# Kernel tuning notes

Measured on AMD Instinct MI355X. Metric: run time of the kernel, lower is better.

Reference implementation:

```python
import jax, jax.numpy as jnp
import numpy as np

NUM_NODES = 17185
D = 6
FEATS = NUM_NODES * D  # 103110
BATCH = 256
EPS = 1e-5


def setup_inputs() -> dict:
    key = jax.random.key(0)
    ks = jax.random.split(key, 4)
    data = jax.random.normal(ks[0], (BATCH, FEATS), dtype=jnp.float32)
    w_blocks = jax.random.normal(ks[1], (NUM_NODES, D, D), dtype=jnp.float32) * (1.0 / np.sqrt(D))
    b_blocks = jax.random.normal(ks[2], (NUM_NODES, D), dtype=jnp.float32) * 0.1
    fc_w = jax.random.normal(ks[3], (FEATS,), dtype=jnp.float32) * (1.0 / np.sqrt(FEATS))
    return {
        "data": data,
        "w_blocks": w_blocks,
        "b_blocks": b_blocks,
        "bn_gamma": jnp.ones((FEATS,), jnp.float32),
        "bn_beta": jnp.zeros((FEATS,), jnp.float32),
        "bn_mean": jnp.zeros((FEATS,), jnp.float32),
        "bn_var": jnp.ones((FEATS,), jnp.float32),
        "fc_w": fc_w,
        "fc_b": jnp.zeros((1,), jnp.float32),
        "bnf_gamma": jnp.ones((1,), jnp.float32),
        "bnf_beta": jnp.zeros((1,), jnp.float32),
        "bnf_mean": jnp.zeros((1,), jnp.float32),
        "bnf_var": jnp.ones((1,), jnp.float32),
    }


def reference(data, w_blocks, b_blocks, bn_gamma, bn_beta, bn_mean, bn_var,
              fc_w, fc_b, bnf_gamma, bnf_beta, bnf_mean, bnf_var):
    B = data.shape[0]
    # block-diagonal batched matmul replacing 17185 tiny Linear(6,6) calls
    x = data.reshape(B, NUM_NODES, D)                       # [B, N, 6]
    xo = jnp.einsum("bni,noi->bno", x, w_blocks) + b_blocks  # torch Linear: x @ W^T + b
    xo = xo.reshape(B, FEATS)                               # hstack ordering == reshape
    # relu -> BatchNorm1d (eval: running stats) -> dropout (identity in eval)
    h = jnp.maximum(xo, 0.0)
    h = (h - bn_mean) * jax.lax.rsqrt(bn_var + EPS) * bn_gamma + bn_beta
    # final linear [FEATS -> 1], BN(1), sigmoid
    y = h @ fc_w + fc_b                                     # [B]
    y = y[:, None]                                          # [B, 1]
    y = (y - bnf_mean) * jax.lax.rsqrt(bnf_var + EPS) * bnf_gamma + bnf_beta
    return jax.nn.sigmoid(y)
```

## Files before the change

kernel.cpp:

```cpp
#include <hip/hip_runtime.h>
#include <stdint.h>

#define NUM_NODES 17185
#define DD 6
#define FEATS (NUM_NODES * DD)
#define BATCH 256
#define EPS 1e-5f

#define NC 256
#define BC 16
#define NCHUNK ((NUM_NODES + NC - 1) / NC)


__global__ __launch_bounds__(NC) void main_kernel(
    const float* __restrict__ data, const float* __restrict__ wb, const float* __restrict__ bb,
    const float* __restrict__ gamma, const float* __restrict__ var, const float* __restrict__ fcw,
    const float* __restrict__ beta, const float* __restrict__ mean,
    float* __restrict__ pm, float* __restrict__ pc) {

    const int tid = threadIdx.x;
    const int n = blockIdx.x * NC + tid;
    const bool valid = (n < NUM_NODES);

    float wreg[36], bias[6], a[6];
    #pragma unroll
    for (int k = 0; k < 36; k++) wreg[k] = 0.f;
    #pragma unroll
    for (int k = 0; k < 6; k++) { bias[k] = 0.f; a[k] = 0.f; }

    float cnode = 0.f;

    if (valid) {
        const float4* wp = (const float4*)(wb + (size_t)n * 36);
        #pragma unroll
        for (int k = 0; k < 9; k++) {
            float4 v = wp[k];
            wreg[4*k] = v.x; wreg[4*k+1] = v.y; wreg[4*k+2] = v.z; wreg[4*k+3] = v.w;
        }
        const float2* bp = (const float2*)(bb + (size_t)n * 6);
        #pragma unroll
        for (int k = 0; k < 3; k++) { float2 v = bp[k]; bias[2*k] = v.x; bias[2*k+1] = v.y; }
        const int f0 = n * 6;
        const float2* gp = (const float2*)(gamma + f0);
        const float2* vp = (const float2*)(var + f0);
        const float2* fp = (const float2*)(fcw + f0);
        float fw[6];
        #pragma unroll
        for (int k = 0; k < 3; k++) {
            float2 g = gp[k], v = vp[k], f = fp[k];
            fw[2*k] = f.x; fw[2*k+1] = f.y;
            a[2*k]   = g.x * rsqrtf(v.x + EPS) * f.x;
            a[2*k+1] = g.y * rsqrtf(v.y + EPS) * f.y;
        }
        if (blockIdx.y == 0) {
            const float2* bep = (const float2*)(beta + f0);
            const float2* mp  = (const float2*)(mean + f0);
            #pragma unroll
            for (int k = 0; k < 3; k++) {
                float2 be = bep[k], m = mp[k];
                cnode += be.x * fw[2*k]   - m.x * a[2*k];
                cnode += be.y * fw[2*k+1] - m.y * a[2*k+1];
            }
        }
    }

    const int b0 = blockIdx.y * BC;
    float acc[BC];
    #pragma unroll
    for (int r = 0; r < BC; r++) acc[r] = 0.f;

    if (valid) {
        const float2* xbase = (const float2*)(data + (size_t)b0 * FEATS + (size_t)n * 6);
        #pragma unroll
        for (int r = 0; r < BC; r++) {
            const float2* xp = xbase + (size_t)r * (FEATS / 2);
            float2 u0 = xp[0], u1 = xp[1], u2 = xp[2];
            float x0 = u0.x, x1 = u0.y, x2 = u1.x, x3 = u1.y, x4 = u2.x, x5 = u2.y;
            #pragma unroll
            for (int o = 0; o < 6; o++) {
                float s = bias[o];
                s = fmaf(x0, wreg[o*6+0], s);
                s = fmaf(x1, wreg[o*6+1], s);
                s = fmaf(x2, wreg[o*6+2], s);
                s = fmaf(x3, wreg[o*6+3], s);
                s = fmaf(x4, wreg[o*6+4], s);
                s = fmaf(x5, wreg[o*6+5], s);
                acc[r] = fmaf(fmaxf(s, 0.f), a[o], acc[r]);
            }
        }
    }

    __shared__ float red[4][BC];
    #pragma unroll
    for (int r = 0; r < BC; r++) {
        float v = acc[r];
        #pragma unroll
        for (int off = 32; off; off >>= 1) v += __shfl_down(v, off);
        if ((tid & 63) == 0) red[tid >> 6][r] = v;
    }

    if (blockIdx.y == 0) {
        float v = cnode;
        #pragma unroll
        for (int off = 32; off; off >>= 1) v += __shfl_down(v, off);
        __shared__ float credd[4];
        if ((tid & 63) == 0) credd[tid >> 6] = v;
        __syncthreads();
        if (tid == 0) pc[blockIdx.x] = credd[0] + credd[1] + credd[2] + credd[3];
    } else {
        __syncthreads();
    }

    if (tid < BC) {
        float s = red[0][tid] + red[1][tid] + red[2][tid] + red[3][tid];
        pm[blockIdx.x * 256 + b0 + tid] = s;
    }
}

__global__ __launch_bounds__(256) void final_kernel(
    const float* __restrict__ pm, const float* __restrict__ pc,
    const float* __restrict__ fcb, const float* __restrict__ bnfg,
    const float* __restrict__ bnfb, const float* __restrict__ bnfm,
    const float* __restrict__ bnfv, float* __restrict__ out) {
    const int b = threadIdx.x;

    float c = (b < NCHUNK) ? pc[b] : 0.f;
    #pragma unroll
    for (int off = 32; off; off >>= 1) c += __shfl_down(c, off);
    __shared__ float red[4];
    if ((b & 63) == 0) red[b >> 6] = c;
    __syncthreads();
    const float c_sum = red[0] + red[1] + red[2] + red[3];

    float y = 0.f;
    #pragma unroll 4
    for (int ch = 0; ch < NCHUNK; ch++) y += pm[ch * 256 + b];

    y += c_sum + fcb[0];
    float sc = bnfg[0] * rsqrtf(bnfv[0] + EPS);
    float z = (y - bnfm[0]) * sc + bnfb[0];
    out[b] = 1.f / (1.f + expf(-z));
}

extern "C" void kernel_launch(void* const* d_in, const int* in_sizes, int n_in,
                              void* d_out, int out_size, void* d_ws, size_t ws_size,
                              hipStream_t stream) {
    const float* data  = (const float*)d_in[0];
    const float* wb    = (const float*)d_in[1];
    const float* bb    = (const float*)d_in[2];
    const float* gamma = (const float*)d_in[3];
    const float* beta  = (const float*)d_in[4];
    const float* mean  = (const float*)d_in[5];
    const float* var   = (const float*)d_in[6];
    const float* fcw   = (const float*)d_in[7];
    const float* fcb   = (const float*)d_in[8];
    const float* bnfg  = (const float*)d_in[9];
    const float* bnfb  = (const float*)d_in[10];
    const float* bnfm  = (const float*)d_in[11];
    const float* bnfv  = (const float*)d_in[12];

    float* pm = (float*)d_ws;
    float* pc = pm + NCHUNK * 256;

    dim3 grid(NCHUNK, BATCH / BC);
    main_kernel<<<grid, NC, 0, stream>>>(data, wb, bb, gamma, var, fcw, beta, mean, pm, pc);

    final_kernel<<<1, 256, 0, stream>>>(pm, pc, fcb, bnfg, bnfb, bnfm, bnfv, (float*)d_out);
}
```

Baseline: 191.5 us.

## Add prep kernel for coalesced weights and stage data rows through swizzled LDS

A new prep kernel folds the BN scale and fc weights into per-node coefficients. It writes the weights, bias and folded coefficients into a global scratch buffer in structure-of-arrays float4 layout, so the main kernel reads them with coalesced loads. The main kernel now loads data rows with fully coalesced float2 accesses into a double-buffered, XOR-swizzled LDS tile, two rows per step, with register prefetch of the next rows. The goal is to replace the strided 24-byte-per-thread global reads. The cost is an extra kernel launch, extra scratch traffic and more barriers.

After: 201.7 us. 1.05x slower.

```diff
diff --git a/kernel.cpp b/kernel.cpp
--- a/kernel.cpp
+++ b/kernel.cpp
@@ -10,71 +10,137 @@
 #define NC 256
 #define BC 16
 #define NCHUNK ((NUM_NODES + NC - 1) / NC)
-
-
-__global__ __launch_bounds__(NC) void main_kernel(
-    const float* __restrict__ data, const float* __restrict__ wb, const float* __restrict__ bb,
-    const float* __restrict__ gamma, const float* __restrict__ var, const float* __restrict__ fcw,
-    const float* __restrict__ beta, const float* __restrict__ mean,
-    float* __restrict__ pm, float* __restrict__ pc) {
-
-    const int tid = threadIdx.x;
-    const int n = blockIdx.x * NC + tid;
+#define ROW_F2 (FEATS / 2)
+#define CHUNK_F2 768
+#define NIT (BC / 2)
+
+__device__ float4 g_W4[NCHUNK * 9 * 256];
+__device__ float4 g_P4[NCHUNK * 3 * 256];
+
+__device__ __forceinline__ int sw2(int i) { return i ^ (((i >> 4) & 7) << 1); }
+
+__global__ __launch_bounds__(256) void prep_kernel(
+    const float* __restrict__ wb, const float* __restrict__ bb,
+    const float* __restrict__ gamma, const float* __restrict__ var,
+    const float* __restrict__ fcw, const float* __restrict__ beta,
+    const float* __restrict__ mean, float* __restrict__ pc) {
+    const int t = threadIdx.x, c = blockIdx.x;
+    const int n = c * NC + t;
     const bool valid = (n < NUM_NODES);
 
-    float wreg[36], bias[6], a[6];
-    #pragma unroll
-    for (int k = 0; k < 36; k++) wreg[k] = 0.f;
-    #pragma unroll
-    for (int k = 0; k < 6; k++) { bias[k] = 0.f; a[k] = 0.f; }
-
-    float cnode = 0.f;
+    float w[36], bi[6], av[6];
+    #pragma unroll
+    for (int k = 0; k < 36; k++) w[k] = 0.f;
+    #pragma unroll
+    for (int k = 0; k < 6; k++) { bi[k] = 0.f; av[k] = 0.f; }
+    float cn = 0.f;
 
     if (valid) {
         const float4* wp = (const float4*)(wb + (size_t)n * 36);
         #pragma unroll
         for (int k = 0; k < 9; k++) {
             float4 v = wp[k];
-            wreg[4*k] = v.x; wreg[4*k+1] = v.y; wreg[4*k+2] = v.z; wreg[4*k+3] = v.w;
+            w[4*k] = v.x; w[4*k+1] = v.y; w[4*k+2] = v.z; w[4*k+3] = v.w;
         }
         const float2* bp = (const float2*)(bb + (size_t)n * 6);
         #pragma unroll
-        for (int k = 0; k < 3; k++) { float2 v = bp[k]; bias[2*k] = v.x; bias[2*k+1] = v.y; }
+        for (int k = 0; k < 3; k++) { float2 v = bp[k]; bi[2*k] = v.x; bi[2*k+1] = v.y; }
         const int f0 = n * 6;
-        const float2* gp = (const float2*)(gamma + f0);
-        const float2* vp = (const float2*)(var + f0);
-        const float2* fp = (const float2*)(fcw + f0);
-        float fw[6];
+        const float2* gp  = (const float2*)(gamma + f0);
+        const float2* vp  = (const float2*)(var + f0);
+        const float2* fp  = (const float2*)(fcw + f0);
+        const float2* bep = (const float2*)(beta + f0);
+        const float2* mp  = (const float2*)(mean + f0);
         #pragma unroll
         for (int k = 0; k < 3; k++) {
-            float2 g = gp[k], v = vp[k], f = fp[k];
-            fw[2*k] = f.x; fw[2*k+1] = f.y;
-            a[2*k]   = g.x * rsqrtf(v.x + EPS) * f.x;
-            a[2*k+1] = g.y * rsqrtf(v.y + EPS) * f.y;
-        }
-        if (blockIdx.y == 0) {
-            const float2* bep = (const float2*)(beta + f0);
-            const float2* mp  = (const float2*)(mean + f0);
+            float2 g = gp[k], v = vp[k], f = fp[k], be = bep[k], m = mp[k];
+            float a0 = g.x * rsqrtf(v.x + EPS) * f.x;
+            float a1 = g.y * rsqrtf(v.y + EPS) * f.y;
+            av[2*k] = a0; av[2*k+1] = a1;
+            cn += be.x * f.x - m.x * a0;
+            cn += be.y * f.y - m.y * a1;
+        }
+    }
+
+    float4* W4 = g_W4 + c * (9 * 256) + t;
+    #pragma unroll
+    for (int j = 0; j < 9; j++)
+        W4[j * 256] = make_float4(w[4*j], w[4*j+1], w[4*j+2], w[4*j+3]);
+    float4* P4 = g_P4 + c * (3 * 256) + t;
+    #pragma unroll
+    for (int k = 0; k < 3; k++)
+        P4[k * 256] = make_float4(bi[2*k], bi[2*k+1], av[2*k], av[2*k+1]);
+
+    #pragma unroll
+    for (int off = 32; off; off >>= 1) cn += __shfl_down(cn, off);
+    __shared__ float credd[4];
+    if ((t & 63) == 0) credd[t >> 6] = cn;
+    __syncthreads();
+    if (t == 0) pc[c] = credd[0] + credd[1] + credd[2] + credd[3];
+}
+
+__global__ __launch_bounds__(256) void main_kernel(
+    const float* __restrict__ data, float* __restrict__ pm) {
+    const int t = threadIdx.x, c = blockIdx.x;
+    const int b0 = blockIdx.y * BC;
+
+    float wreg[36], bias[6], a6[6];
+    {
+        const float4* W4 = g_W4 + c * (9 * 256) + t;
+        #pragma unroll
+        for (int j = 0; j < 9; j++) {
+            float4 v = W4[j * 256];
+            wreg[4*j] = v.x; wreg[4*j+1] = v.y; wreg[4*j+2] = v.z; wreg[4*j+3] = v.w;
+        }
+        const float4* P4 = g_P4 + c * (3 * 256) + t;
+        #pragma unroll
+        for (int k = 0; k < 3; k++) {
+            float4 v = P4[k * 256];
+            bias[2*k] = v.x; bias[2*k+1] = v.y; a6[2*k] = v.z; a6[2*k+1] = v.w;
+        }
+    }
+
+    __shared__ float2 lds2[2 * 1536];
+    const int maxf2 = (c == NCHUNK - 1) ? (ROW_F2 - c * CHUNK_F2) : CHUNK_F2;
+    const float2* dbase = (const float2*)data + (size_t)c * CHUNK_F2;
+
+    float acc[BC];
+    #pragma unroll
+    for (int r = 0; r < BC; r++) acc[r] = 0.f;
+
+    float2 st[6];
+    #pragma unroll
+    for (int k = 0; k < 6; k++) {
+        const int rr = (k >= 3);
+        const int off = t + 256 * (k - 3 * rr);
+        st[k] = (off < maxf2) ? dbase[(size_t)(b0 + rr) * ROW_F2 + off]
+                              : make_float2(0.f, 0.f);
+    }
+    #pragma unroll
+    for (int k = 0; k < 6; k++) {
+        const int idx = t + 256 * k;
+        lds2[sw2(idx)] = st[k];
+    }
+    __syncthreads();
+
+    #pragma unroll
+    for (int it = 0; it < NIT; ++it) {
+        if (it < NIT - 1) {
             #pragma unroll
-            for (int k = 0; k < 3; k++) {
-                float2 be = bep[k], m = mp[k];
-                cnode += be.x * fw[2*k]   - m.x * a[2*k];
-                cnode += be.y * fw[2*k+1] - m.y * a[2*k+1];
+            for (int k = 0; k < 6; k++) {
+                const int rr = (k >= 3);
+                const int off = t + 256 * (k - 3 * rr);
+                st[k] = (off < maxf2)
+                      ? dbase[(size_t)(b0 + 2 * (it + 1) + rr) * ROW_F2 + off]
+                      : make_float2(0.f, 0.f);
             }
         }
-    }
-
-    const int b0 = blockIdx.y * BC;
-    float acc[BC];
-    #pragma unroll
-    for (int r = 0; r < BC; r++) acc[r] = 0.f;
-
-    if (valid) {
-        const float2* xbase = (const float2*)(data + (size_t)b0 * FEATS + (size_t)n * 6);
-        #pragma unroll
-        for (int r = 0; r < BC; r++) {
-            const float2* xp = xbase + (size_t)r * (FEATS / 2);
-            float2 u0 = xp[0], u1 = xp[1], u2 = xp[2];
+        #pragma unroll
+        for (int r2 = 0; r2 < 2; r2++) {
+            const int base = (it & 1) * 1536 + 768 * r2 + 3 * t;
+            float2 u0 = lds2[sw2(base)];
+            float2 u1 = lds2[sw2(base + 1)];
+            float2 u2 = lds2[sw2(base + 2)];
             float x0 = u0.x, x1 = u0.y, x2 = u1.x, x3 = u1.y, x4 = u2.x, x5 = u2.y;
             #pragma unroll
             for (int o = 0; o < 6; o++) {
@@ -85,9 +151,17 @@
                 s = fmaf(x3, wreg[o*6+3], s);
                 s = fmaf(x4, wreg[o*6+4], s);
                 s = fmaf(x5, wreg[o*6+5], s);
-                acc[r] = fmaf(fmaxf(s, 0.f), a[o], acc[r]);
+                acc[2*it + r2] = fmaf(fmaxf(s, 0.f), a6[o], acc[2*it + r2]);
             }
         }
+        if (it < NIT - 1) {
+            #pragma unroll
+            for (int k = 0; k < 6; k++) {
+                const int idx = ((it + 1) & 1) * 1536 + t + 256 * k;
+                lds2[sw2(idx)] = st[k];
+            }
+        }
+        __syncthreads();
     }
 
     __shared__ float red[4][BC];
@@ -96,24 +170,12 @@
         float v = acc[r];
         #pragma unroll
         for (int off = 32; off; off >>= 1) v += __shfl_down(v, off);
-        if ((tid & 63) == 0) red[tid >> 6][r] = v;
-    }
-
-    if (blockIdx.y == 0) {
-        float v = cnode;
-        #pragma unroll
-        for (int off = 32; off; off >>= 1) v += __shfl_down(v, off);
-        __shared__ float credd[4];
-        if ((tid & 63) == 0) credd[tid >> 6] = v;
-        __syncthreads();
-        if (tid == 0) pc[blockIdx.x] = credd[0] + credd[1] + credd[2] + credd[3];
-    } else {
-        __syncthreads();
-    }
-
-    if (tid < BC) {
-        float s = red[0][tid] + red[1][tid] + red[2][tid] + red[3][tid];
-        pm[blockIdx.x * 256 + b0 + tid] = s;
+        if ((t & 63) == 0) red[t >> 6][r] = v;
+    }
+    __syncthreads();
+    if (t < BC) {
+        float s = red[0][t] + red[1][t] + red[2][t] + red[3][t];
+        pm[c * 256 + b0 + t] = s;
     }
 }
 
@@ -162,8 +224,10 @@
     float* pm = (float*)d_ws;
     float* pc = pm + NCHUNK * 256;
 
+    prep_kernel<<<NCHUNK, 256, 0, stream>>>(wb, bb, gamma, var, fcw, beta, mean, pc);
+
     dim3 grid(NCHUNK, BATCH / BC);
-    main_kernel<<<grid, NC, 0, stream>>>(data, wb, bb, gamma, var, fcw, beta, mean, pm, pc);
+    main_kernel<<<grid, NC, 0, stream>>>(data, pm);
 
     final_kernel<<<1, 256, 0, stream>>>(pm, pc, fcb, bnfg, bnfb, bnfm, bnfv, (float*)d_out);
 }
```
